# Performance work log

Hardware: AMD Instinct MI355X
Metric: run time of the kernel (lower is better)

The kernel has to match this reference:

```python
import jax, jax.numpy as jnp
import numpy as np
from jax.scipy.special import i0e

NCELLS = 64
NP = 8
WIDTH_TRAN = 0.5
WIDTH = 3.0
NSAMPLES = 128


def setup_inputs() -> dict:
    key = jax.random.key(0)
    k1, _ = jax.random.split(key)
    # coordinates in [0, 20] so typical pair distances are O(1)-O(10)
    Rin = jax.random.uniform(k1, (NSAMPLES, NCELLS, NP), dtype=jnp.float32) * 20.0
    std = jnp.ones((4,), dtype=jnp.float32)
    bias = jnp.zeros((4,), dtype=jnp.float32)
    return {"Rin": Rin, "std": std, "bias": bias}


def reference(Rin, std, bias):
    Ns = Rin.shape[0]
    R = Rin.reshape(Ns, -1)                      # (Ns, N)
    N = R.shape[1]
    # all-pairs |R_j - R_i|; entry [s, i, j]
    D = jnp.abs(R[:, None, :] - R[:, :, None])   # (Ns, N, N)
    eye = jnp.eye(N, dtype=bool)
    Dsafe = jnp.where(eye, 1.0, D)               # avoid 0 on diagonal (excluded pairs)
    window = 1.0 - 0.5 * jax.lax.erfc(Dsafe / WIDTH_TRAN - WIDTH)
    inv = 1.0 / Dsafe
    # four kernel bases, stacked on last axis: (Ns, N, N, 4)
    basis = jnp.stack([
        window * inv,
        window * jnp.sqrt(inv),
        window * jnp.square(inv),
        window * i0e(Dsafe),
    ], axis=-1)
    mask = (~eye).astype(basis.dtype)            # zero out i == j pairs
    summed = jnp.sum(basis * mask[None, :, :, None], axis=2)  # (Ns, N, 4)
    # original subtracts bias per pair before the sum over the N-1 pairs
    out = jnp.abs(std)[None, None, :] * (summed - (N - 1) * bias[None, None, :])
    return out
```

## Files before the change

### kernel.cpp

```cpp
#include <hip/hip_runtime.h>
#include <math.h>

#define NSAMP 128
#define NTOT  512
#define NJQ   4
#define JCH   (NTOT / NJQ)
#define ITILE 64

#define TBL_N 4096
#define TBL_LAST (TBL_N)
#define TBL_SCALE 204.8f

__device__ float2 g_tbl[TBL_N + 1];


template <int N>
__device__ __forceinline__ float horner(float x, const float (&c)[N]) {
  float p = 0.0f;
#pragma unroll
  for (int i = 0; i < N; ++i) p = __fadd_rn(__fmul_rn(p, x), c[i]);
  return p;
}

template <int N>
__device__ __forceinline__ float chbevl(float x, const float (&c)[N]) {
  float b0 = 0.0f, b1 = 0.0f, b2 = 0.0f;
#pragma unroll
  for (int i = 0; i < N; ++i) {
    b2 = b1;
    b1 = b0;
    b0 = __fadd_rn(__fsub_rn(__fmul_rn(x, b1), b2), c[i]);
  }
  return __fmul_rn(0.5f, __fsub_rn(b0, b2));
}

__device__ __forceinline__ float erfc_xla(float x) {
  const float kErfT[7] = {
      +7.853861353153693E-5f, -8.010193625184903E-4f, +5.188327685732524E-3f,
      -2.685381193529856E-2f, +1.128358514861418E-1f, -3.761262582423300E-1f,
      +1.128379165726710E+0f};
  const float kP[9] = {
      +2.326819970068386E-2f, -1.387039388740657E-1f, +3.687424674597105E-1f,
      -5.824733027278666E-1f, +6.210004621745983E-1f, -4.944515323274145E-1f,
      +3.404879937665872E-1f, -2.741127028184656E-1f, +5.638259427386472E-1f};
  const float kR[8] = {
      -1.047766399936249E+1f, +1.297719955372516E+1f, -7.495518717768503E+0f,
      +2.921019019210786E+0f, -1.015265279202700E+0f, +4.218463358204948E-1f,
      -2.820767439740514E-1f, +5.641895067754075E-1f};

  float ax = fabsf(x);
  float x2 = __fmul_rn(x, x);
  float erf_small = __fmul_rn(x, horner(x2, kErfT));
  float erf_based = __fsub_rn(1.0f, erf_small);
  float z = expf(-x2);
  float q = __fdiv_rn(1.0f, ax);
  float y = __fmul_rn(q, q);
  float p = (ax < 2.0f) ? horner(y, kP) : horner(y, kR);
  float r = __fmul_rn(__fmul_rn(z, q), p);
  float ec = (x < 0.0f) ? __fsub_rn(2.0f, r) : r;
  return (ax < 1.0f) ? erf_based : ec;
}

__device__ __forceinline__ float i0e_xla(float x) {
  const float kA[18] = {
      -1.30002500998624804212E-8f, 6.04699502254191894932E-8f,
      -2.67079385394061173391E-7f, 1.11738753912010371815E-6f,
      -4.41673835845875056359E-6f, 1.64484480707288970893E-5f,
      -5.75419501008210370398E-5f, 1.88502885095841655729E-4f,
      -5.76375574538582365885E-4f, 1.63947561694133579842E-3f,
      -4.32430999505057594430E-3f, 1.05464603945949983183E-2f,
      -2.37374148058994688156E-2f, 4.93052842396707084878E-2f,
      -9.49010970480476444210E-2f, 1.71620901522208775349E-1f,
      -3.04682672343198398683E-1f, 6.76795274409476084995E-1f};
  const float kB[7] = {
      3.39623202570838634515E-9f, 2.26666899049817806459E-8f,
      2.04891858946906374183E-7f, 2.89137052083475648297E-6f,
      6.88975834691682398426E-5f, 3.36911647825569408990E-3f,
      8.04490411014108831608E-1f};
  float le8 = chbevl(__fsub_rn(__fmul_rn(0.5f, x), 2.0f), kA);
  float arg = __fsub_rn(__fdiv_rn(32.0f, x), 2.0f);
  float gt8 = __fdiv_rn(chbevl(arg, kB), __fsqrt_rn(x));
  return (x <= 8.0f) ? le8 : gt8;
}


__global__ __launch_bounds__(256) void fill_tbl_kernel() {
  int k = blockIdx.x * 256 + threadIdx.x;
  if (k > TBL_LAST) return;
  float d = (float)k * (20.0f / (float)TBL_N);
  float t = 2.0f * d - 3.0f;
  float w = 1.0f - 0.5f * erfc_xla(t);
  float io = (k == 0) ? 1.0f : i0e_xla(d);
  g_tbl[k] = make_float2(w, io);
}


__global__ __launch_bounds__(256) void fmm_window_kernel(
    const float* __restrict__ R, const float* __restrict__ stdp,
    const float* __restrict__ biasp, float* __restrict__ out) {
  __shared__ float Rs[NTOT];
  __shared__ float2 T[TBL_N + 1];

  const int tid = threadIdx.x;
  const int bid = blockIdx.x;
  const int s = bid >> 3;
  const int itile = bid & 7;

  for (int k = tid; k <= TBL_LAST; k += 256) T[k] = g_tbl[k];
  Rs[tid] = R[s * NTOT + tid];
  Rs[tid + 256] = R[s * NTOT + tid + 256];
  __syncthreads();

  const int il = tid >> 2;
  const int jq = tid & 3;
  const int i = itile * ITILE + il;
  const float ri = Rs[i];

  float a0 = 0.0f, a1 = 0.0f, a2 = 0.0f, a3 = 0.0f;

  const int jbase = jq * JCH;
#pragma unroll 4
  for (int jj = 0; jj < JCH; jj += 4) {
    const float4 rj = *reinterpret_cast<const float4*>(&Rs[jbase + jj]);
#pragma unroll
    for (int u = 0; u < 4; ++u) {
      const float rjv = (u == 0) ? rj.x : (u == 1) ? rj.y : (u == 2) ? rj.z : rj.w;
      const float d = fabsf(rjv - ri);
      const float x = d * TBL_SCALE;
      const int k = (int)x;
      const float f = x - (float)k;
      const float2 t0 = T[k];
      const float2 t1 = T[k + 1];
      float w = fmaf(f, t1.x - t0.x, t0.x);
      const float io = fmaf(f, t1.y - t0.y, t0.y);
      const bool z = (d == 0.0f);
      const float dd = z ? 1.0f : d;
      w = z ? 0.0f : w;
      const float inv = __builtin_amdgcn_rcpf(dd);
      const float rsq = __builtin_amdgcn_rsqf(dd);
      a0 = fmaf(w, inv, a0);
      a1 = fmaf(w, rsq, a1);
      a2 = fmaf(w * inv, inv, a2);
      a3 = fmaf(w, io, a3);
    }
  }

  a0 += __shfl_xor(a0, 1);  a0 += __shfl_xor(a0, 2);
  a1 += __shfl_xor(a1, 1);  a1 += __shfl_xor(a1, 2);
  a2 += __shfl_xor(a2, 1);  a2 += __shfl_xor(a2, 2);
  a3 += __shfl_xor(a3, 1);  a3 += __shfl_xor(a3, 2);

  if (jq == 0) {
    float* o = out + ((size_t)(s * NTOT + i)) * 4;
    const float nm1 = 511.0f;
    o[0] = fabsf(stdp[0]) * (a0 - nm1 * biasp[0]);
    o[1] = fabsf(stdp[1]) * (a1 - nm1 * biasp[1]);
    o[2] = fabsf(stdp[2]) * (a2 - nm1 * biasp[2]);
    o[3] = fabsf(stdp[3]) * (a3 - nm1 * biasp[3]);
  }
}

extern "C" void kernel_launch(void* const* d_in, const int* in_sizes, int n_in,
                              void* d_out, int out_size, void* d_ws, size_t ws_size,
                              hipStream_t stream) {
  const float* R = (const float*)d_in[0];
  const float* stdp = (const float*)d_in[1];
  const float* biasp = (const float*)d_in[2];
  float* out = (float*)d_out;

  hipLaunchKernelGGL(fill_tbl_kernel, dim3((TBL_N + 256) / 256), dim3(256), 0,
                     stream);
  hipLaunchKernelGGL(fmm_window_kernel, dim3(NSAMP * (NTOT / ITILE)), dim3(256),
                     0, stream, R, stdp, biasp, out);
}
```

Before: 90.09 us.

## Shrink lookup table to float4 value+slope entries and use 512-thread blocks

Replaces the 4097-entry float2 table with a 1026-entry float4 table holding value and slope, so each pair does one LDS read instead of two and the per-block table copy is smaller. Blocks grow to 512 threads, splitting j across 8 lanes with padded shared R to avoid bank conflicts, plus a third shuffle step in the reduction. It also uses hardware fract and a fmax guard in place of the select. The coarser table spacing raises interpolation error for the window and i0e terms.

```diff
diff --git a/kernel.cpp b/kernel.cpp
--- a/kernel.cpp
+++ b/kernel.cpp
@@ -3,15 +3,16 @@
 
 #define NSAMP 128
 #define NTOT  512
-#define NJQ   4
+#define NJQ   8
 #define JCH   (NTOT / NJQ)
 #define ITILE 64
 
-#define TBL_N 4096
-#define TBL_LAST (TBL_N)
-#define TBL_SCALE 204.8f
+#define TBL_N    1024
+#define TBL_SIZE (TBL_N + 2)
+#define TBL_H    0.01953125f
+#define TBL_SCALE 51.2f
 
-__device__ float2 g_tbl[TBL_N + 1];
+__device__ float4 g_tbl[TBL_SIZE];
 
 
 template <int N>
@@ -83,72 +84,79 @@
   return (x <= 8.0f) ? le8 : gt8;
 }
 
+__device__ __forceinline__ float window_ref(float d) {
+  return 1.0f - 0.5f * erfc_xla(2.0f * d - 3.0f);
+}
+
 
 __global__ __launch_bounds__(256) void fill_tbl_kernel() {
   int k = blockIdx.x * 256 + threadIdx.x;
-  if (k > TBL_LAST) return;
-  float d = (float)k * (20.0f / (float)TBL_N);
-  float t = 2.0f * d - 3.0f;
-  float w = 1.0f - 0.5f * erfc_xla(t);
-  float io = (k == 0) ? 1.0f : i0e_xla(d);
-  g_tbl[k] = make_float2(w, io);
+  if (k >= TBL_SIZE) return;
+  float d0 = fminf((float)k * TBL_H, 20.0f);
+  float d1 = fminf(d0 + TBL_H, 20.0f);
+  float w0 = window_ref(d0);
+  float w1 = window_ref(d1);
+  float io0 = i0e_xla(d0);
+  float io1 = i0e_xla(d1);
+  g_tbl[k] = make_float4(w0, w1 - w0, io0, io1 - io0);
 }
 
 
-__global__ __launch_bounds__(256) void fmm_window_kernel(
+#define RSP(j) ((j) + (((j) >> 6) << 2))
+#define RSP_SIZE (NTOT + 4 * (NJQ - 1))
+
+__global__ __launch_bounds__(512) void fmm_window_kernel(
     const float* __restrict__ R, const float* __restrict__ stdp,
     const float* __restrict__ biasp, float* __restrict__ out) {
-  __shared__ float Rs[NTOT];
-  __shared__ float2 T[TBL_N + 1];
+  __shared__ float4 T[TBL_SIZE];
+  __shared__ float Rs[RSP_SIZE];
 
   const int tid = threadIdx.x;
   const int bid = blockIdx.x;
   const int s = bid >> 3;
   const int itile = bid & 7;
 
-  for (int k = tid; k <= TBL_LAST; k += 256) T[k] = g_tbl[k];
-  Rs[tid] = R[s * NTOT + tid];
-  Rs[tid + 256] = R[s * NTOT + tid + 256];
+  for (int k = tid; k < TBL_SIZE; k += 512) T[k] = g_tbl[k];
+  Rs[RSP(tid)] = R[s * NTOT + tid];
   __syncthreads();
 
-  const int il = tid >> 2;
-  const int jq = tid & 3;
+  const int il = tid >> 3;
+  const int jq = tid & 7;
   const int i = itile * ITILE + il;
-  const float ri = Rs[i];
+  const float ri = Rs[RSP(i)];
 
   float a0 = 0.0f, a1 = 0.0f, a2 = 0.0f, a3 = 0.0f;
 
-  const int jbase = jq * JCH;
+  const int jw = jq * 68;
 #pragma unroll 4
   for (int jj = 0; jj < JCH; jj += 4) {
-    const float4 rj = *reinterpret_cast<const float4*>(&Rs[jbase + jj]);
+    const float4 rj = *reinterpret_cast<const float4*>(&Rs[jw + jj]);
 #pragma unroll
     for (int u = 0; u < 4; ++u) {
       const float rjv = (u == 0) ? rj.x : (u == 1) ? rj.y : (u == 2) ? rj.z : rj.w;
       const float d = fabsf(rjv - ri);
       const float x = d * TBL_SCALE;
       const int k = (int)x;
-      const float f = x - (float)k;
-      const float2 t0 = T[k];
-      const float2 t1 = T[k + 1];
-      float w = fmaf(f, t1.x - t0.x, t0.x);
-      const float io = fmaf(f, t1.y - t0.y, t0.y);
-      const bool z = (d == 0.0f);
-      const float dd = z ? 1.0f : d;
-      w = z ? 0.0f : w;
+      const float f = __builtin_amdgcn_fractf(x);
+      const float4 tv = T[k];
+      float w = fmaf(f, tv.y, tv.x);
+      const float io = fmaf(f, tv.w, tv.z);
+      w = (d == 0.0f) ? 0.0f : w;
+      const float dd = fmaxf(d, 1e-30f);
       const float inv = __builtin_amdgcn_rcpf(dd);
       const float rsq = __builtin_amdgcn_rsqf(dd);
+      const float wi = w * inv;
       a0 = fmaf(w, inv, a0);
       a1 = fmaf(w, rsq, a1);
-      a2 = fmaf(w * inv, inv, a2);
+      a2 = fmaf(wi, inv, a2);
       a3 = fmaf(w, io, a3);
     }
   }
 
-  a0 += __shfl_xor(a0, 1);  a0 += __shfl_xor(a0, 2);
-  a1 += __shfl_xor(a1, 1);  a1 += __shfl_xor(a1, 2);
-  a2 += __shfl_xor(a2, 1);  a2 += __shfl_xor(a2, 2);
-  a3 += __shfl_xor(a3, 1);  a3 += __shfl_xor(a3, 2);
+  a0 += __shfl_xor(a0, 1); a0 += __shfl_xor(a0, 2); a0 += __shfl_xor(a0, 4);
+  a1 += __shfl_xor(a1, 1); a1 += __shfl_xor(a1, 2); a1 += __shfl_xor(a1, 4);
+  a2 += __shfl_xor(a2, 1); a2 += __shfl_xor(a2, 2); a2 += __shfl_xor(a2, 4);
+  a3 += __shfl_xor(a3, 1); a3 += __shfl_xor(a3, 2); a3 += __shfl_xor(a3, 4);
 
   if (jq == 0) {
     float* o = out + ((size_t)(s * NTOT + i)) * 4;
@@ -168,8 +176,8 @@
   const float* biasp = (const float*)d_in[2];
   float* out = (float*)d_out;
 
-  hipLaunchKernelGGL(fill_tbl_kernel, dim3((TBL_N + 256) / 256), dim3(256), 0,
-                     stream);
-  hipLaunchKernelGGL(fmm_window_kernel, dim3(NSAMP * (NTOT / ITILE)), dim3(256),
+  hipLaunchKernelGGL(fill_tbl_kernel, dim3((TBL_SIZE + 255) / 256), dim3(256),
+                     0, stream);
+  hipLaunchKernelGGL(fmm_window_kernel, dim3(NSAMP * (NTOT / ITILE)), dim3(512),
                      0, stream, R, stdp, biasp, out);
 }
```

Measured after the change: 76.95 us. -14.6%, faster.
